# Optimization experiments

Hardware: AMD Instinct MI355X
Metric: run time of the kernel (lower is better)

## Reference

```python
import jax, jax.numpy as jnp
import numpy as np


def setup_inputs() -> dict:
    key = jax.random.key(0)
    k1, k2 = jax.random.split(key)
    B, L, D = 16, 512, 256
    text_features = jax.random.normal(k1, (B, L, D), dtype=jnp.float32)
    durations = jax.random.randint(k2, (B, L), 0, 32, dtype=jnp.int64)
    return {"text_features": text_features, "durations": durations, "target_length": 8192}


def reference(text_features, durations, target_length):
    """Length-regulator: expand [B,L,d] phoneme features to [B,T,d] frames.

    Frame t of batch b copies phoneme p where cumsum(dur)[b,p-1] <= t < cumsum(dur)[b,p];
    frames past the total duration are zero (matches torch zeros-init + trim/pad to
    target_length, since padding with the last frame only occurs when the buffer was
    already target_length long in the original code path with target_length set).
    """
    B, L, D = text_features.shape
    T = target_length  # static python int -> jit-friendly fixed output length
    cum = jnp.cumsum(durations, axis=1)                      # [B, L]
    t = jnp.arange(T, dtype=cum.dtype)                       # [T]
    # first phoneme index p with cum[b,p] > t  (side='right')
    idx = jax.vmap(lambda c: jnp.searchsorted(c, t, side='right'))(cum)  # [B, T]
    idx = jnp.minimum(idx, L - 1)
    valid = t[None, :] < cum[:, -1:]                         # [B, T] frames within total dur
    gathered = jnp.take_along_axis(text_features, idx[:, :, None], axis=1)  # [B, T, D]
    return jnp.where(valid[:, :, None], gathered, jnp.zeros((), dtype=text_features.dtype))
```

## Files before the change

### kernel.cpp

```cpp
#include <hip/hip_runtime.h>

#define MAX_L 2048
#define MAX_EPC 8
#define FPB 128

__global__ __launch_bounds__(256) void lr_fused_kernel(
        const float* __restrict__ feat,
        const int* __restrict__ dur,
        const int* __restrict__ tlen,
        float* __restrict__ out,
        int BL, int BT, int D) {
    const int T = *tlen;
    const int B = BT / T;
    const int L = BL / B;
    const int vecs = D >> 2;

    __shared__ int sc[MAX_L];
    __shared__ int swsum[4];
    __shared__ int sidx[FPB];

    const long frame_base0 = (long)blockIdx.x * FPB;
    if (frame_base0 >= BT) return;

    const int tid  = threadIdx.x;
    const int lane = tid & 63;
    const int wv   = tid >> 6;

    long fb_ = frame_base0;
    int remaining = (int)((long)BT - frame_base0 < FPB ? (long)BT - frame_base0
                                                       : (long)FPB);

    while (remaining > 0) {
        const int b   = (int)(fb_ / T);
        const int tt0 = (int)(fb_ - (long)b * T);
        const int seg = remaining < (T - tt0) ? remaining : (T - tt0);

        __syncthreads();
        const int epc  = (L + blockDim.x - 1) / blockDim.x;
        const int base = tid * epc;
        const int* __restrict__ drow = dur + (size_t)b * L;
        int local[MAX_EPC];
        int run = 0;
#pragma unroll
        for (int e = 0; e < MAX_EPC; ++e) {
            int v = 0;
            if (e < epc && base + e < L) v = drow[base + e];
            run += v;
            local[e] = run;
        }
        int wsum = run;
#pragma unroll
        for (int off = 1; off < 64; off <<= 1) {
            int up = __shfl_up(wsum, off, 64);
            if (lane >= off) wsum += up;
        }
        if (lane == 63) swsum[wv] = wsum;
        __syncthreads();
        int wprefix = 0;
        for (int w = 0; w < wv; ++w) wprefix += swsum[w];
        const int chunk_prefix = wprefix + wsum - run;
#pragma unroll
        for (int e = 0; e < MAX_EPC; ++e)
            if (e < epc && base + e < L) sc[base + e] = chunk_prefix + local[e];
        __syncthreads();

        const int total = sc[L - 1];

        if (tid < seg) {
            const int t = tt0 + tid;
            int p = -1;
            if (t < total) {
                int lo = 0, hi = L - 1;
                while (lo < hi) {
                    const int mid = (lo + hi) >> 1;
                    if (sc[mid] > t) hi = mid;
                    else             lo = mid + 1;
                }
                p = lo;
            }
            sidx[tid] = p;
        }
        __syncthreads();

        if (seg == FPB && vecs == 64) {
            const float4* __restrict__ fbp =
                (const float4*)feat + (size_t)b * L * 64;
            float4* __restrict__ op =
                (float4*)out + ((size_t)fb_ + (size_t)wv * 32) * 64 + lane;
            const int si = sidx[wv * 32 + (lane & 31)];
            int prev = -2;
            float4 v = make_float4(0.f, 0.f, 0.f, 0.f);
#pragma unroll
            for (int j = 0; j < 32; ++j) {
                const int p = __builtin_amdgcn_readlane(si, j);
                if (p != prev) {
                    v = (p >= 0) ? fbp[(size_t)p * 64 + lane]
                                 : make_float4(0.f, 0.f, 0.f, 0.f);
                    prev = p;
                }
                op[(size_t)j * 64] = v;
            }
        } else {
            const float4* __restrict__ fbp =
                (const float4*)feat + (size_t)b * L * vecs;
            const float4 z = make_float4(0.f, 0.f, 0.f, 0.f);
            for (int f = wv; f < seg; f += 4) {
                const int p = sidx[f];
                float4* __restrict__ orow = (float4*)out + ((size_t)fb_ + f) * vecs;
                if (p >= 0) {
                    const float4* __restrict__ irow = fbp + (size_t)p * vecs;
                    for (int i = lane; i < vecs; i += 64) orow[i] = irow[i];
                } else {
                    for (int i = lane; i < vecs; i += 64) orow[i] = z;
                }
            }
        }

        fb_ += seg;
        remaining -= seg;
    }
}

extern "C" void kernel_launch(void* const* d_in, const int* in_sizes, int n_in,
                              void* d_out, int out_size, void* d_ws, size_t ws_size,
                              hipStream_t stream) {
    const float* feat = (const float*)d_in[0];
    const int*   dur  = (const int*)d_in[1];
    const int*   tlen = (const int*)d_in[2];

    const int BL = in_sizes[1];
    const int D  = in_sizes[0] / in_sizes[1];
    const int BT = out_size / D;

    const int grid = (BT + FPB - 1) / FPB;
    lr_fused_kernel<<<grid, 256, 0, stream>>>(feat, dur, tlen, (float*)d_out,
                                              BL, BT, D);
}
```

Measured before the change: 145.8 us.

## Split into index-map kernel and copy kernel to avoid per-block cumsum

```diff
diff --git a/kernel.cpp b/kernel.cpp
--- a/kernel.cpp
+++ b/kernel.cpp
@@ -3,6 +3,115 @@
 #define MAX_L 2048
 #define MAX_EPC 8
 #define FPB 128
+
+__global__ __launch_bounds__(256) void lr_index_kernel(
+        const int* __restrict__ dur,
+        const int* __restrict__ tlen,
+        int* __restrict__ gmap,
+        int BL, int BT) {
+    const int T = *tlen;
+    const int B = BT / T;
+    const int L = BL / B;
+
+    __shared__ int sc[MAX_L];
+    __shared__ int swsum[4];
+
+    const int tid  = threadIdx.x;
+    const int lane = tid & 63;
+    const int wv   = tid >> 6;
+
+    for (int b = blockIdx.x; b < B; b += gridDim.x) {
+        __syncthreads();
+
+        const int epc  = (L + blockDim.x - 1) / blockDim.x;
+        const int base = tid * epc;
+        const int* __restrict__ drow = dur + (size_t)b * L;
+        int local[MAX_EPC];
+        int run = 0;
+#pragma unroll
+        for (int e = 0; e < MAX_EPC; ++e) {
+            int v = 0;
+            if (e < epc && base + e < L) v = drow[base + e];
+            run += v;
+            local[e] = run;
+        }
+        int wsum = run;
+#pragma unroll
+        for (int off = 1; off < 64; off <<= 1) {
+            int up = __shfl_up(wsum, off, 64);
+            if (lane >= off) wsum += up;
+        }
+        if (lane == 63) swsum[wv] = wsum;
+        __syncthreads();
+        int wprefix = 0;
+        for (int w = 0; w < wv; ++w) wprefix += swsum[w];
+        const int chunk_prefix = wprefix + wsum - run;
+#pragma unroll
+        for (int e = 0; e < MAX_EPC; ++e)
+            if (e < epc && base + e < L) sc[base + e] = chunk_prefix + local[e];
+        __syncthreads();
+
+        const int total_raw = sc[L - 1];
+        const int total = total_raw < T ? total_raw : T;
+        int* __restrict__ gm = gmap + (size_t)b * T;
+
+        for (int p = tid; p < L; p += blockDim.x) {
+            int s = p ? sc[p - 1] : 0;
+            int e = sc[p];
+            if (s > T) s = T;
+            if (e > T) e = T;
+            const int g = b * L + p;
+            for (int t = s; t < e; ++t) gm[t] = g;
+        }
+        for (int t = total + tid; t < T; t += blockDim.x) gm[t] = -1;
+    }
+}
+
+__global__ __launch_bounds__(256) void lr_copy_kernel(
+        const float* __restrict__ feat,
+        const int* __restrict__ gmap,
+        float* __restrict__ out,
+        int BT, int vecs) {
+    const long fb = (long)blockIdx.x * FPB;
+    if (fb >= BT) return;
+
+    const int tid  = threadIdx.x;
+    const int lane = tid & 63;
+    const int wv   = tid >> 6;
+    const int nf   = (int)(((long)BT - fb) < FPB ? ((long)BT - fb) : (long)FPB);
+
+    if (nf == FPB && vecs == 64) {
+        const long f0 = fb + (long)wv * 32;
+        const int si = gmap[f0 + (lane & 31)];
+        const float4* __restrict__ fv = (const float4*)feat;
+        float4* __restrict__ op = (float4*)out + (size_t)f0 * 64 + lane;
+        int prev = -2;
+        float4 v = make_float4(0.f, 0.f, 0.f, 0.f);
+#pragma unroll
+        for (int j = 0; j < 32; ++j) {
+            const int g = __builtin_amdgcn_readlane(si, j);
+            if (g != prev) {
+                v = (g >= 0) ? fv[(size_t)g * 64 + lane]
+                             : make_float4(0.f, 0.f, 0.f, 0.f);
+                prev = g;
+            }
+            op[(size_t)j * 64] = v;
+        }
+    } else {
+        const float4 z = make_float4(0.f, 0.f, 0.f, 0.f);
+        for (int f = wv; f < nf; f += 4) {
+            const int g = gmap[fb + f];
+            float4* __restrict__ orow = (float4*)out + (size_t)(fb + f) * vecs;
+            if (g >= 0) {
+                const float4* __restrict__ irow =
+                    (const float4*)feat + (size_t)g * vecs;
+                for (int i = lane; i < vecs; i += 64) orow[i] = irow[i];
+            } else {
+                for (int i = lane; i < vecs; i += 64) orow[i] = z;
+            }
+        }
+    }
+}
 
 __global__ __launch_bounds__(256) void lr_fused_kernel(
         const float* __restrict__ feat,
@@ -133,6 +242,13 @@
     const int BT = out_size / D;
 
     const int grid = (BT + FPB - 1) / FPB;
-    lr_fused_kernel<<<grid, 256, 0, stream>>>(feat, dur, tlen, (float*)d_out,
-                                              BL, BT, D);
-}
+
+    if (ws_size >= (size_t)BT * sizeof(int)) {
+        lr_index_kernel<<<64, 256, 0, stream>>>(dur, tlen, (int*)d_ws, BL, BT);
+        lr_copy_kernel<<<grid, 256, 0, stream>>>(feat, (int*)d_ws,
+                                                 (float*)d_out, BT, D >> 2);
+    } else {
+        lr_fused_kernel<<<grid, 256, 0, stream>>>(feat, dur, tlen, (float*)d_out,
+                                                  BL, BT, D);
+    }
+}
```

After: 149.1 us. 2.3% more time.
